# Kernel tuning notes

Hardware: AMD Instinct MI355X
Metric: run time of the kernel (lower is better)

The kernel has to match this reference:

```python
import jax, jax.numpy as jnp
import numpy as np

B, S, D, H, MB = 2, 2048, 2048, 32, 16
HD = D // H          # 64
N = S // MB          # 128 mini-batches
EPS = 1e-5
BASE_LR = 1.0


def setup_inputs() -> dict:
    ks = jax.random.split(jax.random.key(0), 8)
    sc = 1.0 / np.sqrt(D)
    inv = 1.0 / (10000.0 ** (np.arange(0, HD, 2, dtype=np.float64) / HD))
    return {
        "x": jax.random.normal(ks[0], (B, S, D), jnp.float32),
        "pos_frequencies": jnp.asarray(np.outer(np.arange(S), inv), jnp.float32),  # (S, HD//2) rope angles
        "Wq": jax.random.normal(ks[1], (D, D), jnp.float32) * sc,
        "Wk": jax.random.normal(ks[2], (D, D), jnp.float32) * sc,
        "Wv": jax.random.normal(ks[3], (D, D), jnp.float32) * sc,
        "Wo": jax.random.normal(ks[4], (D, D), jnp.float32) * sc,
        "post_gamma": jnp.ones((D,), jnp.float32),
        "post_beta": jnp.zeros((D,), jnp.float32),
        "ilr_W": jax.random.normal(ks[5], (H, 1, D), jnp.float32) * 0.02,  # inner_loop_lr_W
        "ilr_b": jnp.zeros((H, 1), jnp.float32),                            # inner_loop_lr_b
        "lgs": jnp.zeros((MB,), jnp.float32),                               # learnable_gradient_scale
        "ttt_gamma": jnp.ones((H, HD), jnp.float32),                        # ttt_norm_weight
        "ttt_beta": jnp.zeros((H, HD), jnp.float32),                        # ttt_norm_bias
        "W0": jax.random.normal(ks[6], (H, HD, HD), jnp.float32) / np.sqrt(HD),
        "b0": jnp.zeros((H, 1, HD), jnp.float32),
    }


def _rope(x, freqs):
    # x: (B,H,S,HD), freqs: (S,HD//2); rotate interleaved pairs
    cos = jnp.cos(freqs)[None, None]
    sin = jnp.sin(freqs)[None, None]
    x1, x2 = x[..., 0::2], x[..., 1::2]
    return jnp.stack([x1 * cos - x2 * sin, x1 * sin + x2 * cos], -1).reshape(x.shape)


def _ln_fwd(z, g, b):
    mu = z.mean(-1, keepdims=True)
    var = z.var(-1, keepdims=True)
    return g * (z - mu) * jax.lax.rsqrt(var + EPS) + b


def _ln_l2_bwd(z, tgt, g, b):
    # grad of 0.5*||LN(z) - tgt||^2 w.r.t. z (fused LayerNorm backward)
    mu = z.mean(-1, keepdims=True)
    var = z.var(-1, keepdims=True)
    rstd = jax.lax.rsqrt(var + EPS)
    zh = (z - mu) * rstd
    dy = (g * zh + b) - tgt
    dzh = dy * g
    return (dzh - dzh.mean(-1, keepdims=True) - zh * (dzh * zh).mean(-1, keepdims=True)) * rstd


def reference(x, pos_frequencies, Wq, Wk, Wv, Wo, post_gamma, post_beta,
              ilr_W, ilr_b, lgs, ttt_gamma, ttt_beta, W0, b0):
    # projections (torch Linear: x @ W.T), shape (B,H,S,HD)
    q = (x @ Wq.T).reshape(B, S, H, HD).transpose(0, 2, 1, 3)
    k = (x @ Wk.T).reshape(B, S, H, HD).transpose(0, 2, 1, 3)
    v = (x @ Wv.T).reshape(B, S, H, HD).transpose(0, 2, 1, 3)
    q = _rope(q, pos_frequencies)
    k = _rope(k, pos_frequencies)
    v = _rope(v, pos_frequencies)  # module applies RoPE to V too

    # inner-loop learning rates: (B,H,N,1,MB), gradient_scale: (MB,1)
    xr = x.reshape(B, N, MB, D)
    lr = jnp.einsum('bnkd,hod->bhnko', xr, ilr_W) + ilr_b.reshape(1, H, 1, 1, 1)
    lr = BASE_LR * jax.nn.sigmoid(lr).transpose(0, 1, 2, 4, 3) / HD
    gs = jnp.clip(1.0 / jnp.arange(1, MB + 1, dtype=jnp.float32) + lgs, 0.0)
    eta = gs.reshape(1, 1, 1, MB, 1) * lr  # (B,H,N,MB,MB)

    to_n = lambda t: t.reshape(B, H, N, MB, -1).transpose(2, 0, 1, 3, 4)
    Qn, Kn, Vn = to_n(q), to_n(k), to_n(v)           # (N,B,H,MB,HD)
    En = eta.transpose(2, 0, 1, 3, 4)                # (N,B,H,MB,MB)

    g = ttt_gamma.reshape(1, H, 1, HD)
    be = ttt_beta.reshape(1, H, 1, HD)
    W_init = jnp.broadcast_to(W0[None], (B, H, HD, HD))
    b_init = jnp.broadcast_to(b0[None], (B, H, 1, HD))

    def step(carry, inp):
        W, bb = carry
        XQ, XK, XV, E = inp
        Z = XK @ W + bb
        grad = _ln_l2_bwd(Z, XV - XK, g, be)                 # (B,H,MB,HD)
        Attn = jnp.tril(XQ @ XK.swapaxes(-1, -2))            # causal dual form
        b_bar = bb - jnp.tril(E) @ grad
        Z_bar = XQ @ W - (E * Attn) @ grad + b_bar
        last_eta = E[..., -1, :, None]                       # (B,H,MB,1)
        W_new = W - jnp.swapaxes(last_eta * XK, -1, -2) @ grad
        b_new = bb - jnp.sum(last_eta * grad, axis=-2, keepdims=True)
        return (W_new, b_new), XQ + _ln_fwd(Z_bar, g, be)

    _, ys = jax.lax.scan(step, (W_init, b_init), (Qn, Kn, Vn, En))  # ys: (N,B,H,MB,HD)
    out = ys.transpose(1, 0, 3, 2, 4).reshape(B, S, D)

    mu = out.mean(-1, keepdims=True)
    var = out.var(-1, keepdims=True)
    out = post_gamma * (out - mu) * jax.lax.rsqrt(var + EPS) + post_beta
    return out @ Wo.T
```

## Files before the change

### kernel.cpp

```cpp
#include <hip/hip_runtime.h>
#include <hip/hip_bf16.h>
#include <math.h>

#define BB 2
#define SS 2048
#define DD 2048
#define HH 32
#define HDD 64
#define MBB 16
#define NN 128

typedef unsigned short u16;
typedef short bf16x8_t __attribute__((ext_vector_type(8)));
typedef float f32x4_t __attribute__((ext_vector_type(4)));

__device__ __forceinline__ float b2f(u16 u) { return __uint_as_float(((unsigned)u) << 16); }
__device__ __forceinline__ u16 f2b(float f) {
    unsigned u = __float_as_uint(f);
    return (u16)((u + 0x7FFFu + ((u >> 16) & 1u)) >> 16);
}
__device__ __forceinline__ unsigned pk2(float a, float b) {
    return (unsigned)f2b(a) | ((unsigned)f2b(b) << 16);
}
__device__ __forceinline__ unsigned pk2r(u16 a, u16 b) { return (unsigned)a | ((unsigned)b << 16); }
__device__ __forceinline__ float wsum(float x) {
    x += __shfl_xor(x, 32);
    x += __shfl_xor(x, 16);
    x += __shfl_xor(x, 8);
    x += __shfl_xor(x, 4);
    x += __shfl_xor(x, 2);
    x += __shfl_xor(x, 1);
    return x;
}

typedef __attribute__((address_space(3))) unsigned int lds_u32;
typedef __attribute__((address_space(1))) const unsigned int glb_u32;
__device__ __forceinline__ void async_copy16(const void* g, void* l) {
    __builtin_amdgcn_global_load_lds((glb_u32*)g, (lds_u32*)l, 16, 0, 0);
}

__global__ __launch_bounds__(256) void k_cvt5(const float* __restrict__ x, const float* __restrict__ wq,
                                              const float* __restrict__ wk, const float* __restrict__ wv,
                                              const float* __restrict__ wo, u16* __restrict__ xb,
                                              u16* __restrict__ wqb, u16* __restrict__ wkb,
                                              u16* __restrict__ wvb, u16* __restrict__ wob) {
    int sl = blockIdx.y;
    long e = (long)(blockIdx.x * 256 + threadIdx.x) * 4;
    const float* s;
    u16* d;
    if (sl == 0) { s = x; d = xb; }
    else if (sl == 1) { s = x + 4194304; d = xb + 4194304; }
    else if (sl == 2) { s = wq; d = wqb; }
    else if (sl == 3) { s = wk; d = wkb; }
    else if (sl == 4) { s = wv; d = wvb; }
    else { s = wo; d = wob; }
    float4 f = *(const float4*)(s + e);
    uint2 o;
    o.x = pk2(f.x, f.y);
    o.y = pk2(f.z, f.w);
    *(uint2*)(d + e) = o;
}

__global__ void k_trig(const float* __restrict__ pf, float* __restrict__ ct, float* __restrict__ st) {
    int i = blockIdx.x * 256 + threadIdx.x;
    float f = pf[i];
    ct[i] = cosf(f);
    st[i] = sinf(f);
}

template <int EPI>
__global__ __launch_bounds__(256) void k_gemm_bt(const u16* __restrict__ A, const u16* __restrict__ B0,
                                                 const u16* __restrict__ B1, const u16* __restrict__ B2,
                                                 void* __restrict__ C0, void* __restrict__ C1,
                                                 void* __restrict__ C2, int M, int Nn, int K,
                                                 const float* __restrict__ ct, const float* __restrict__ st) {
    __shared__ u16 As[128 * 32];
    __shared__ u16 Bs[128 * 32];
    int z = blockIdx.z;
    const u16* Bm = (z == 0) ? B0 : (z == 1) ? B1 : B2;
    void* Cout = (z == 0) ? C0 : (z == 1) ? C1 : C2;
    int tid = threadIdx.x, lane = tid & 63, wv = tid >> 6;
    int m0 = blockIdx.y * 128, n0 = blockIdx.x * 128;
    int wm = wv >> 1, wn = wv & 1;

    f32x4_t acc[4][4];
    f32x4_t zero = {0.f, 0.f, 0.f, 0.f};
#pragma unroll
    for (int a = 0; a < 4; ++a)
#pragma unroll
        for (int b = 0; b < 4; ++b) acc[a][b] = zero;

    int mrow = lane & 15, qk = (lane >> 4) * 8;
    const int kTiles = K >> 5;
    for (int kt = 0; kt < kTiles; ++kt) {
        __syncthreads();
        int kb = kt << 5;
#pragma unroll
        for (int it = 0; it < 2; ++it) {
            int cb = it * 256 + wv * 64;
            int c = cb + lane;
            const u16* gpA = A + (m0 + (c >> 2)) * K + kb + ((c & 3) << 3);
            async_copy16(gpA, &As[cb << 3]);
            const u16* gpB = Bm + (n0 + (c >> 2)) * K + kb + ((c & 3) << 3);
            async_copy16(gpB, &Bs[cb << 3]);
        }
        asm volatile("s_waitcnt vmcnt(0)" ::: "memory");
        __syncthreads();

        bf16x8_t af[4], bfr[4];
#pragma unroll
        for (int mi = 0; mi < 4; ++mi)
            af[mi] = *(const bf16x8_t*)&As[(wm * 64 + mi * 16 + mrow) * 32 + qk];
#pragma unroll
        for (int ni = 0; ni < 4; ++ni)
            bfr[ni] = *(const bf16x8_t*)&Bs[(wn * 64 + ni * 16 + mrow) * 32 + qk];
#pragma unroll
        for (int mi = 0; mi < 4; ++mi)
#pragma unroll
            for (int ni = 0; ni < 4; ++ni)
                acc[mi][ni] = __builtin_amdgcn_mfma_f32_16x16x32_bf16(af[mi], bfr[ni], acc[mi][ni], 0, 0, 0);
    }

    int col16 = lane & 15, rq = (lane >> 4) * 4;
#pragma unroll
    for (int mi = 0; mi < 4; ++mi) {
#pragma unroll
        for (int ni = 0; ni < 4; ++ni) {
#pragma unroll
            for (int r = 0; r < 4; ++r) {
                int gr = m0 + wm * 64 + mi * 16 + rq + r;
                int gc = n0 + wn * 64 + ni * 16 + col16;
                float val = acc[mi][ni][r];
                if (EPI == 0) {
                    ((float*)Cout)[gr * Nn + gc] = val;
                } else {
                    int b = gr >> 11, s2 = gr & 2047, hh = gc >> 6, hd = gc & 63;
                    int fi = s2 * 32 + (hd >> 1);
                    float c = ct[fi], sn = st[fi];
                    float partner = __shfl_xor(val, 1);
                    float y = (gc & 1) ? (partner * sn + val * c) : (val * c - partner * sn);
                    ((u16*)Cout)[(((b * HH + hh) * SS) + s2) * HDD + hd] = f2b(y);
                }
            }
        }
    }
}

__global__ __launch_bounds__(256) void k_lr(const u16* __restrict__ xb, const float* __restrict__ ilrW,
                                            const float* __restrict__ ilrb, float* __restrict__ lrout) {
    __shared__ u16 xr[4][2048];
    int row0 = blockIdx.x * 4;
    int tid = threadIdx.x, lane = tid & 63, wv = tid >> 6;
    const unsigned* src = (const unsigned*)(xb + row0 * 2048);
    unsigned* dst = (unsigned*)xr;
    for (int i = tid; i < 4096; i += 256) dst[i] = src[i];
    __syncthreads();
    int b = row0 >> 11, s0 = row0 & 2047;
#pragma unroll
    for (int sub = 0; sub < 8; ++sub) {
        int h = wv * 8 + sub;
        const float* wp = ilrW + h * 2048;
        float a0 = 0.f, a1 = 0.f, a2 = 0.f, a3 = 0.f;
        for (int i = 0; i < 16; ++i) {
            int idx = i * 128 + lane * 2;
            float2 w2 = *(const float2*)(wp + idx);
            unsigned p0 = *(const unsigned*)&xr[0][idx];
            unsigned p1 = *(const unsigned*)&xr[1][idx];
            unsigned p2 = *(const unsigned*)&xr[2][idx];
            unsigned p3 = *(const unsigned*)&xr[3][idx];
            a0 += b2f((u16)p0) * w2.x + b2f((u16)(p0 >> 16)) * w2.y;
            a1 += b2f((u16)p1) * w2.x + b2f((u16)(p1 >> 16)) * w2.y;
            a2 += b2f((u16)p2) * w2.x + b2f((u16)(p2 >> 16)) * w2.y;
            a3 += b2f((u16)p3) * w2.x + b2f((u16)(p3 >> 16)) * w2.y;
        }
        a0 = wsum(a0);
        a1 = wsum(a1);
        a2 = wsum(a2);
        a3 = wsum(a3);
        if (lane == 0) {
            float bv = ilrb[h];
            float* op = lrout + ((b * HH + h) * SS) + s0;
            op[0] = (1.0f / (1.0f + expf(-(a0 + bv)))) * (1.0f / 64.0f);
            op[1] = (1.0f / (1.0f + expf(-(a1 + bv)))) * (1.0f / 64.0f);
            op[2] = (1.0f / (1.0f + expf(-(a2 + bv)))) * (1.0f / 64.0f);
            op[3] = (1.0f / (1.0f + expf(-(a3 + bv)))) * (1.0f / 64.0f);
        }
    }
}

__global__ __launch_bounds__(64) void k_scan(const u16* __restrict__ qb, const u16* __restrict__ kb2,
                                             const u16* __restrict__ vb, const float* __restrict__ lrbuf,
                                             const float* __restrict__ lgs, const float* __restrict__ tg,
                                             const float* __restrict__ tb, const float* __restrict__ W0,
                                             const float* __restrict__ b0, u16* __restrict__ ys) {
    __shared__ u16 WbL[64 * 72];
    __shared__ u16 XKT[64 * 40];
    __shared__ u16 GST[64 * 40];
    __shared__ u16 PUL[16 * 40];

    const int bh = blockIdx.x, h = bh & 31, b = bh >> 5;
    const int lane = threadIdx.x & 63;
    const int quad = lane >> 4, col = lane & 15;
    const int base = bh * SS;

    {
        unsigned* p1 = (unsigned*)XKT;
        unsigned* p2 = (unsigned*)GST;
        unsigned* p3 = (unsigned*)PUL;
        for (int i = lane; i < 1280; i += 64) { p1[i] = 0; p2[i] = 0; }
        for (int i = lane; i < 320; i += 64) p3[i] = 0;
    }

    float gd4[4], bd4[4], bbv[4];
#pragma unroll
    for (int tn = 0; tn < 4; ++tn) {
        gd4[tn] = tg[h * 64 + tn * 16 + col];
        bd4[tn] = tb[h * 64 + tn * 16 + col];
        bbv[tn] = b0[h * 64 + tn * 16 + col];
    }
    float gs4[4];
#pragma unroll
    for (int r = 0; r < 4; ++r) {
        int i = quad * 4 + r;
        gs4[r] = fmaxf(1.f / (float)(i + 1) + lgs[i], 0.f);
    }
    const float gs15 = fmaxf(1.f / 16.f + lgs[15], 0.f);

    f32x4_t Wc[4][4];
#pragma unroll
    for (int tm = 0; tm < 4; ++tm)
#pragma unroll
        for (int tn = 0; tn < 4; ++tn)
#pragma unroll
            for (int r = 0; r < 4; ++r)
                Wc[tm][tn][r] = W0[h * 4096 + (tm * 16 + quad * 4 + r) * 64 + tn * 16 + col];

    {
        unsigned* wb32 = (unsigned*)WbL;
#pragma unroll
        for (int tn = 0; tn < 4; ++tn)
#pragma unroll
            for (int tm = 0; tm < 4; ++tm) {
                int a = (tn * 16 + col) * 36 + tm * 4 + quad;
                a = (tn * 16 + col) * 36 + tm * 8 + quad * 2;
                wb32[a] = pk2(Wc[tm][tn][0], Wc[tm][tn][1]);
                wb32[a + 1] = pk2(Wc[tm][tn][2], Wc[tm][tn][3]);
            }
    }

    bf16x8_t ka[2], qa[2];
    float lr4[4];
    u16 kraw[16], vraw[16];
    {
        const u16* kp = kb2 + (base + col) * 64;
        const u16* qp = qb + (base + col) * 64;
#pragma unroll
        for (int kh = 0; kh < 2; ++kh) {
            ka[kh] = *(const bf16x8_t*)(kp + kh * 32 + quad * 8);
            qa[kh] = *(const bf16x8_t*)(qp + kh * 32 + quad * 8);
        }
#pragma unroll
        for (int r = 0; r < 4; ++r) lr4[r] = lrbuf[base + quad * 4 + r];
#pragma unroll
        for (int tn = 0; tn < 4; ++tn)
#pragma unroll
            for (int r = 0; r < 4; ++r) {
                int idx = (base + quad * 4 + r) * 64 + tn * 16 + col;
                kraw[tn * 4 + r] = kb2[idx];
                vraw[tn * 4 + r] = vb[idx];
            }
    }

    const f32x4_t zf = {0.f, 0.f, 0.f, 0.f};

    for (int n = 0; n < NN; ++n) {
        const int s0 = n * 16;

        bf16x8_t wbf[4][2];
#pragma unroll
        for (int tn = 0; tn < 4; ++tn)
#pragma unroll
            for (int kh = 0; kh < 2; ++kh)
                wbf[tn][kh] = *(const bf16x8_t*)&WbL[(tn * 16 + col) * 72 + kh * 32 + quad * 8];

        f32x4_t z[4], xqw[4], attn;
#pragma unroll
        for (int tn = 0; tn < 4; ++tn) {
            z[tn] = __builtin_amdgcn_mfma_f32_16x16x32_bf16(ka[1], wbf[tn][1], zf, 0, 0, 0);
            z[tn] = __builtin_amdgcn_mfma_f32_16x16x32_bf16(ka[0], wbf[tn][0], z[tn], 0, 0, 0);
            xqw[tn] = __builtin_amdgcn_mfma_f32_16x16x32_bf16(qa[1], wbf[tn][1], zf, 0, 0, 0);
            xqw[tn] = __builtin_amdgcn_mfma_f32_16x16x32_bf16(qa[0], wbf[tn][0], xqw[tn], 0, 0, 0);
        }
        attn = __builtin_amdgcn_mfma_f32_16x16x32_bf16(qa[1], ka[1], zf, 0, 0, 0);
        attn = __builtin_amdgcn_mfma_f32_16x16x32_bf16(qa[0], ka[0], attn, 0, 0, 0);

        u16 qraw[16];
#pragma unroll
        for (int tn = 0; tn < 4; ++tn)
#pragma unroll
            for (int r = 0; r < 4; ++r)
                qraw[tn * 4 + r] = qb[(base + s0 + quad * 4 + r) * 64 + tn * 16 + col];

        bf16x8_t nka[2], nqa[2];
        float nlr[4];
        u16 nkraw[16], nvraw[16];
        {
            const int sp = (n + 1 < NN) ? s0 + 16 : s0;
            const u16* kp = kb2 + (base + sp + col) * 64;
            const u16* qp = qb + (base + sp + col) * 64;
#pragma unroll
            for (int kh = 0; kh < 2; ++kh) {
                nka[kh] = *(const bf16x8_t*)(kp + kh * 32 + quad * 8);
                nqa[kh] = *(const bf16x8_t*)(qp + kh * 32 + quad * 8);
            }
#pragma unroll
            for (int r = 0; r < 4; ++r) nlr[r] = lrbuf[base + sp + quad * 4 + r];
#pragma unroll
            for (int tn = 0; tn < 4; ++tn)
#pragma unroll
                for (int r = 0; r < 4; ++r) {
                    int idx = (base + sp + quad * 4 + r) * 64 + tn * 16 + col;
                    nkraw[tn * 4 + r] = kb2[idx];
                    nvraw[tn * 4 + r] = vb[idx];
                }
        }

        {
            unsigned* x32 = (unsigned*)XKT;
#pragma unroll
            for (int tn = 0; tn < 4; ++tn) {
                int a = (tn * 16 + col) * 20 + quad * 2;
                x32[a] = pk2r(kraw[tn * 4 + 0], kraw[tn * 4 + 1]);
                x32[a + 1] = pk2r(kraw[tn * 4 + 2], kraw[tn * 4 + 3]);
            }
        }

#pragma unroll
        for (int tn = 0; tn < 4; ++tn)
#pragma unroll
            for (int r = 0; r < 4; ++r) z[tn][r] += bbv[tn];

        float mu4[4], rstd4[4], m1[4], m2[4];
#pragma unroll
        for (int r = 0; r < 4; ++r) {
            float s1 = z[0][r] + z[1][r] + z[2][r] + z[3][r];
            float s2 = z[0][r] * z[0][r] + z[1][r] * z[1][r] + z[2][r] * z[2][r] + z[3][r] * z[3][r];
#pragma unroll
            for (int m = 1; m <= 8; m <<= 1) { s1 += __shfl_xor(s1, m); s2 += __shfl_xor(s2, m); }
            float mu = s1 * (1.f / 64.f);
            float var = s2 * (1.f / 64.f) - mu * mu;
            mu4[r] = mu;
            rstd4[r] = rsqrtf(var + 1e-5f);
            m1[r] = 0.f;
            m2[r] = 0.f;
        }
#pragma unroll
        for (int tn = 0; tn < 4; ++tn)
#pragma unroll
            for (int r = 0; r < 4; ++r) {
                float zh = (z[tn][r] - mu4[r]) * rstd4[r];
                float tgt = b2f(vraw[tn * 4 + r]) - b2f(kraw[tn * 4 + r]);
                float dzh = (gd4[tn] * zh + bd4[tn] - tgt) * gd4[tn];
                m1[r] += dzh;
                m2[r] += dzh * zh;
            }
#pragma unroll
        for (int r = 0; r < 4; ++r) {
#pragma unroll
            for (int m = 1; m <= 8; m <<= 1) { m1[r] += __shfl_xor(m1[r], m); m2[r] += __shfl_xor(m2[r], m); }
            m1[r] *= (1.f / 64.f);
            m2[r] *= (1.f / 64.f);
        }
        float gS[4][4];
#pragma unroll
        for (int tn = 0; tn < 4; ++tn)
#pragma unroll
            for (int r = 0; r < 4; ++r) {
                float zh = (z[tn][r] - mu4[r]) * rstd4[r];
                float tgt = b2f(vraw[tn * 4 + r]) - b2f(kraw[tn * 4 + r]);
                float dzh = (gd4[tn] * zh + bd4[tn] - tgt) * gd4[tn];
                gS[tn][r] = lr4[r] * ((dzh - m1[r] - zh * m2[r]) * rstd4[r]);
            }
        {
            unsigned* g32 = (unsigned*)GST;
#pragma unroll
            for (int tn = 0; tn < 4; ++tn) {
                int a = (tn * 16 + col) * 20 + quad * 2;
                g32[a] = pk2(gS[tn][0], gS[tn][1]);
                g32[a + 1] = pk2(gS[tn][2], gS[tn][3]);
            }
        }
#pragma unroll
        for (int r = 0; r < 4; ++r) {
            float pv = (col <= quad * 4 + r) ? (1.f + attn[r]) : 0.f;
            PUL[(quad * 4 + r) * 40 + col] = f2b(pv);
        }

        bf16x8_t xkf[4], gsf[4], puf;
#pragma unroll
        for (int t = 0; t < 4; ++t) {
            xkf[t] = *(const bf16x8_t*)&XKT[(t * 16 + col) * 40 + quad * 8];
            gsf[t] = *(const bf16x8_t*)&GST[(t * 16 + col) * 40 + quad * 8];
        }
        puf = *(const bf16x8_t*)&PUL[col * 40 + quad * 8];

#pragma unroll
        for (int tm = 0; tm < 4; ++tm)
#pragma unroll
            for (int tn = 0; tn < 4; ++tn) {
                f32x4_t dw = __builtin_amdgcn_mfma_f32_16x16x32_bf16(xkf[tm], gsf[tn], zf, 0, 0, 0);
#pragma unroll
                for (int r = 0; r < 4; ++r) Wc[tm][tn][r] -= gs15 * dw[r];
            }
        {
            unsigned* wb32 = (unsigned*)WbL;
#pragma unroll
            for (int tn = 0; tn < 4; ++tn)
#pragma unroll
                for (int tm = 0; tm < 4; ++tm) {
                    int a = (tn * 16 + col) * 36 + tm * 8 + quad * 2;
                    wb32[a] = pk2(Wc[tm][tn][0], Wc[tm][tn][1]);
                    wb32[a + 1] = pk2(Wc[tm][tn][2], Wc[tm][tn][3]);
                }
        }

#pragma unroll
        for (int tn = 0; tn < 4; ++tn) {
            f32x4_t pg = __builtin_amdgcn_mfma_f32_16x16x32_bf16(puf, gsf[tn], zf, 0, 0, 0);
#pragma unroll
            for (int r = 0; r < 4; ++r) z[tn][r] = xqw[tn][r] + bbv[tn] - gs4[r] * pg[r];
        }
#pragma unroll
        for (int r = 0; r < 4; ++r) {
            float s1 = z[0][r] + z[1][r] + z[2][r] + z[3][r];
            float s2 = z[0][r] * z[0][r] + z[1][r] * z[1][r] + z[2][r] * z[2][r] + z[3][r] * z[3][r];
#pragma unroll
            for (int m = 1; m <= 8; m <<= 1) { s1 += __shfl_xor(s1, m); s2 += __shfl_xor(s2, m); }
            float mu = s1 * (1.f / 64.f);
            float var = s2 * (1.f / 64.f) - mu * mu;
            mu4[r] = mu;
            rstd4[r] = rsqrtf(var + 1e-5f);
        }
#pragma unroll
        for (int tn = 0; tn < 4; ++tn)
#pragma unroll
            for (int r = 0; r < 4; ++r) {
                float y = b2f(qraw[tn * 4 + r]) + gd4[tn] * (z[tn][r] - mu4[r]) * rstd4[r] + bd4[tn];
                ys[(b * SS + s0 + quad * 4 + r) * DD + h * 64 + tn * 16 + col] = f2b(y);
            }

#pragma unroll
        for (int tn = 0; tn < 4; ++tn) {
            float c = gS[tn][0] + gS[tn][1] + gS[tn][2] + gS[tn][3];
            c += __shfl_xor(c, 16);
            c += __shfl_xor(c, 32);
            bbv[tn] -= gs15 * c;
        }

        ka[0] = nka[0]; ka[1] = nka[1];
        qa[0] = nqa[0]; qa[1] = nqa[1];
#pragma unroll
        for (int r = 0; r < 4; ++r) lr4[r] = nlr[r];
#pragma unroll
        for (int j = 0; j < 16; ++j) { kraw[j] = nkraw[j]; vraw[j] = nvraw[j]; }
    }
}

__global__ __launch_bounds__(256) void k_postln(const u16* __restrict__ ys, const float* __restrict__ pg,
                                                const float* __restrict__ pb, u16* __restrict__ outb) {
    __shared__ float red[8];
    int row = blockIdx.x, tid = threadIdx.x, lane = tid & 63, wv = tid >> 6;
    const u16* rp = ys + row * 2048 + tid * 8;
    uint4 pkd = *(const uint4*)rp;
    float v[8];
    v[0] = b2f((u16)pkd.x); v[1] = b2f((u16)(pkd.x >> 16));
    v[2] = b2f((u16)pkd.y); v[3] = b2f((u16)(pkd.y >> 16));
    v[4] = b2f((u16)pkd.z); v[5] = b2f((u16)(pkd.z >> 16));
    v[6] = b2f((u16)pkd.w); v[7] = b2f((u16)(pkd.w >> 16));
    float s1 = 0.f, s2 = 0.f;
#pragma unroll
    for (int i = 0; i < 8; ++i) { s1 += v[i]; s2 += v[i] * v[i]; }
    s1 = wsum(s1);
    s2 = wsum(s2);
    if (lane == 0) {
        red[wv] = s1;
        red[wv + 4] = s2;
    }
    __syncthreads();
    float S1 = red[0] + red[1] + red[2] + red[3];
    float S2 = red[4] + red[5] + red[6] + red[7];
    float mu = S1 * (1.f / 2048), var = S2 * (1.f / 2048) - mu * mu;
    float rstd = rsqrtf(var + 1e-5f);
    const float4 g0 = *(const float4*)(pg + tid * 8);
    const float4 g1 = *(const float4*)(pg + tid * 8 + 4);
    const float4 b0v = *(const float4*)(pb + tid * 8);
    const float4 b1v = *(const float4*)(pb + tid * 8 + 4);
    float o[8];
    o[0] = g0.x * (v[0] - mu) * rstd + b0v.x;
    o[1] = g0.y * (v[1] - mu) * rstd + b0v.y;
    o[2] = g0.z * (v[2] - mu) * rstd + b0v.z;
    o[3] = g0.w * (v[3] - mu) * rstd + b0v.w;
    o[4] = g1.x * (v[4] - mu) * rstd + b1v.x;
    o[5] = g1.y * (v[5] - mu) * rstd + b1v.y;
    o[6] = g1.z * (v[6] - mu) * rstd + b1v.z;
    o[7] = g1.w * (v[7] - mu) * rstd + b1v.w;
    uint4 po;
    po.x = pk2(o[0], o[1]);
    po.y = pk2(o[2], o[3]);
    po.z = pk2(o[4], o[5]);
    po.w = pk2(o[6], o[7]);
    *(uint4*)(outb + row * 2048 + tid * 8) = po;
}

extern "C" void kernel_launch(void* const* d_in, const int* in_sizes, int n_in,
                              void* d_out, int out_size, void* d_ws, size_t ws_size,
                              hipStream_t stream) {
    const float* x = (const float*)d_in[0];
    const float* pf = (const float*)d_in[1];
    const float* Wq = (const float*)d_in[2];
    const float* Wk = (const float*)d_in[3];
    const float* Wv = (const float*)d_in[4];
    const float* Wo = (const float*)d_in[5];
    const float* pg = (const float*)d_in[6];
    const float* pb = (const float*)d_in[7];
    const float* ilrW = (const float*)d_in[8];
    const float* ilrb = (const float*)d_in[9];
    const float* lgs = (const float*)d_in[10];
    const float* tg = (const float*)d_in[11];
    const float* tb = (const float*)d_in[12];
    const float* W0 = (const float*)d_in[13];
    const float* b0 = (const float*)d_in[14];
    float* out = (float*)d_out;
    char* ws = (char*)d_ws;

    u16* xbf = (u16*)(ws + 0);
    u16* wqb = (u16*)(ws + 16777216);
    u16* wkb = (u16*)(ws + 25165824);
    u16* wvb = (u16*)(ws + 33554432);
    u16* wob = (u16*)(ws + 41943040);
    u16* qbuf = (u16*)(ws + 50331648);
    u16* kbuf = (u16*)(ws + 67108864);
    u16* vbuf = (u16*)(ws + 83886080);
    float* ct = (float*)(ws + 100663296);
    float* st = (float*)(ws + 100925440);
    float* lrb = (float*)(ws + 101187584);
    u16* ysb = (u16*)(ws + 101711872);
    u16* lnb = (u16*)(ws + 0);

    k_cvt5<<<dim3(4096, 6), 256, 0, stream>>>(x, Wq, Wk, Wv, Wo, xbf, wqb, wkb, wvb, wob);
    k_trig<<<256, 256, 0, stream>>>(pf, ct, st);

    k_gemm_bt<1><<<dim3(16, 32, 3), 256, 0, stream>>>(xbf, wqb, wkb, wvb, qbuf, kbuf, vbuf,
                                                      4096, 2048, 2048, ct, st);

    k_lr<<<1024, 256, 0, stream>>>(xbf, ilrW, ilrb, lrb);

    k_scan<<<64, 64, 0, stream>>>(qbuf, kbuf, vbuf, lrb, lgs, tg, tb, W0, b0, ysb);

    k_postln<<<4096, 256, 0, stream>>>(ysb, pg, pb, lnb);
    k_gemm_bt<0><<<dim3(16, 32, 1), 256, 0, stream>>>(lnb, wob, wob, wob, out, out, out,
                                                      4096, 2048, 2048, nullptr, nullptr);
}
```

Before: 853.4 us.

## Pack eight scan heads per workgroup and pad XKT/GST LDS stride

The TTT scan kernel previously launched 64 single-wave workgroups, one per (batch, head). It now launches 8 workgroups of 512 threads, each wave owning a private slice of LDS for its head. The XKT/GST row stride also changes from 40 to 36 elements, and reads are split into two 4-element loads, apparently to reduce LDS bank conflicts. Packing waves onto fewer CUs may cut launch or scheduling overhead, but it concentrates all 64 serial scans onto 8 CUs. That risks contention for MFMA, LDS and VGPR resources and could lengthen the latency-bound serial loop.

```diff
diff --git a/kernel.cpp b/kernel.cpp
--- a/kernel.cpp
+++ b/kernel.cpp
@@ -12,6 +12,7 @@
 
 typedef unsigned short u16;
 typedef short bf16x8_t __attribute__((ext_vector_type(8)));
+typedef short bf16x4_t __attribute__((ext_vector_type(4)));
 typedef float f32x4_t __attribute__((ext_vector_type(4)));
 
 __device__ __forceinline__ float b2f(u16 u) { return __uint_as_float(((unsigned)u) << 16); }
@@ -188,26 +189,32 @@
     }
 }
 
-__global__ __launch_bounds__(64) void k_scan(const u16* __restrict__ qb, const u16* __restrict__ kb2,
-                                             const u16* __restrict__ vb, const float* __restrict__ lrbuf,
-                                             const float* __restrict__ lgs, const float* __restrict__ tg,
-                                             const float* __restrict__ tb, const float* __restrict__ W0,
-                                             const float* __restrict__ b0, u16* __restrict__ ys) {
-    __shared__ u16 WbL[64 * 72];
-    __shared__ u16 XKT[64 * 40];
-    __shared__ u16 GST[64 * 40];
-    __shared__ u16 PUL[16 * 40];
-
-    const int bh = blockIdx.x, h = bh & 31, b = bh >> 5;
+__global__ __launch_bounds__(512) void k_scan(const u16* __restrict__ qb, const u16* __restrict__ kb2,
+                                              const u16* __restrict__ vb, const float* __restrict__ lrbuf,
+                                              const float* __restrict__ lgs, const float* __restrict__ tg,
+                                              const float* __restrict__ tb, const float* __restrict__ W0,
+                                              const float* __restrict__ b0, u16* __restrict__ ys) {
+    __shared__ u16 WbL[8][64 * 72];
+    __shared__ u16 XKT[8][64 * 36];
+    __shared__ u16 GST[8][64 * 36];
+    __shared__ u16 PUL[8][16 * 40];
+
+    const int w = threadIdx.x >> 6;
+    const int bh = blockIdx.x * 8 + w, h = bh & 31, b = bh >> 5;
     const int lane = threadIdx.x & 63;
     const int quad = lane >> 4, col = lane & 15;
     const int base = bh * SS;
 
+    u16* const WbLw = WbL[w];
+    u16* const XKTw = XKT[w];
+    u16* const GSTw = GST[w];
+    u16* const PULw = PUL[w];
+
     {
-        unsigned* p1 = (unsigned*)XKT;
-        unsigned* p2 = (unsigned*)GST;
-        unsigned* p3 = (unsigned*)PUL;
-        for (int i = lane; i < 1280; i += 64) { p1[i] = 0; p2[i] = 0; }
+        unsigned* p1 = (unsigned*)XKTw;
+        unsigned* p2 = (unsigned*)GSTw;
+        unsigned* p3 = (unsigned*)PULw;
+        for (int i = lane; i < 1152; i += 64) { p1[i] = 0; p2[i] = 0; }
         for (int i = lane; i < 320; i += 64) p3[i] = 0;
     }
 
@@ -236,13 +243,12 @@
                 Wc[tm][tn][r] = W0[h * 4096 + (tm * 16 + quad * 4 + r) * 64 + tn * 16 + col];
 
     {
-        unsigned* wb32 = (unsigned*)WbL;
+        unsigned* wb32 = (unsigned*)WbLw;
 #pragma unroll
         for (int tn = 0; tn < 4; ++tn)
 #pragma unroll
             for (int tm = 0; tm < 4; ++tm) {
-                int a = (tn * 16 + col) * 36 + tm * 4 + quad;
-                a = (tn * 16 + col) * 36 + tm * 8 + quad * 2;
+                int a = (tn * 16 + col) * 36 + tm * 8 + quad * 2;
                 wb32[a] = pk2(Wc[tm][tn][0], Wc[tm][tn][1]);
                 wb32[a + 1] = pk2(Wc[tm][tn][2], Wc[tm][tn][3]);
             }
@@ -281,7 +287,7 @@
         for (int tn = 0; tn < 4; ++tn)
 #pragma unroll
             for (int kh = 0; kh < 2; ++kh)
-                wbf[tn][kh] = *(const bf16x8_t*)&WbL[(tn * 16 + col) * 72 + kh * 32 + quad * 8];
+                wbf[tn][kh] = *(const bf16x8_t*)&WbLw[(tn * 16 + col) * 72 + kh * 32 + quad * 8];
 
         f32x4_t z[4], xqw[4], attn;
 #pragma unroll
@@ -326,10 +332,10 @@
         }
 
         {
-            unsigned* x32 = (unsigned*)XKT;
+            unsigned* x32 = (unsigned*)XKTw;
 #pragma unroll
             for (int tn = 0; tn < 4; ++tn) {
-                int a = (tn * 16 + col) * 20 + quad * 2;
+                int a = (tn * 16 + col) * 18 + quad * 2;
                 x32[a] = pk2r(kraw[tn * 4 + 0], kraw[tn * 4 + 1]);
                 x32[a + 1] = pk2r(kraw[tn * 4 + 2], kraw[tn * 4 + 3]);
             }
@@ -382,10 +388,10 @@
                 gS[tn][r] = lr4[r] * ((dzh - m1[r] - zh * m2[r]) * rstd4[r]);
             }
         {
-            unsigned* g32 = (unsigned*)GST;
+            unsigned* g32 = (unsigned*)GSTw;
 #pragma unroll
             for (int tn = 0; tn < 4; ++tn) {
-                int a = (tn * 16 + col) * 20 + quad * 2;
+                int a = (tn * 16 + col) * 18 + quad * 2;
                 g32[a] = pk2(gS[tn][0], gS[tn][1]);
                 g32[a + 1] = pk2(gS[tn][2], gS[tn][3]);
             }
@@ -393,16 +399,20 @@
 #pragma unroll
         for (int r = 0; r < 4; ++r) {
             float pv = (col <= quad * 4 + r) ? (1.f + attn[r]) : 0.f;
-            PUL[(quad * 4 + r) * 40 + col] = f2b(pv);
+            PULw[(quad * 4 + r) * 40 + col] = f2b(pv);
         }
 
         bf16x8_t xkf[4], gsf[4], puf;
 #pragma unroll
         for (int t = 0; t < 4; ++t) {
-            xkf[t] = *(const bf16x8_t*)&XKT[(t * 16 + col) * 40 + quad * 8];
-            gsf[t] = *(const bf16x8_t*)&GST[(t * 16 + col) * 40 + quad * 8];
-        }
-        puf = *(const bf16x8_t*)&PUL[col * 40 + quad * 8];
+            bf16x4_t xl = *(const bf16x4_t*)&XKTw[(t * 16 + col) * 36 + quad * 8];
+            bf16x4_t xh = *(const bf16x4_t*)&XKTw[(t * 16 + col) * 36 + quad * 8 + 4];
+            xkf[t] = __builtin_shufflevector(xl, xh, 0, 1, 2, 3, 4, 5, 6, 7);
+            bf16x4_t gl = *(const bf16x4_t*)&GSTw[(t * 16 + col) * 36 + quad * 8];
+            bf16x4_t gh = *(const bf16x4_t*)&GSTw[(t * 16 + col) * 36 + quad * 8 + 4];
+            gsf[t] = __builtin_shufflevector(gl, gh, 0, 1, 2, 3, 4, 5, 6, 7);
+        }
+        puf = *(const bf16x8_t*)&PULw[col * 40 + quad * 8];
 
 #pragma unroll
         for (int tm = 0; tm < 4; ++tm)
@@ -413,7 +423,7 @@
                 for (int r = 0; r < 4; ++r) Wc[tm][tn][r] -= gs15 * dw[r];
             }
         {
-            unsigned* wb32 = (unsigned*)WbL;
+            unsigned* wb32 = (unsigned*)WbLw;
 #pragma unroll
             for (int tn = 0; tn < 4; ++tn)
 #pragma unroll
@@ -555,7 +565,7 @@
 
     k_lr<<<1024, 256, 0, stream>>>(xbf, ilrW, ilrb, lrb);
 
-    k_scan<<<64, 64, 0, stream>>>(qbuf, kbuf, vbuf, lrb, lgs, tg, tb, W0, b0, ysb);
+    k_scan<<<dim3(8), 512, 0, stream>>>(qbuf, kbuf, vbuf, lrb, lgs, tg, tb, W0, b0, ysb);
 
     k_postln<<<4096, 256, 0, stream>>>(ysb, pg, pb, lnb);
     k_gemm_bt<0><<<dim3(16, 32, 1), 256, 0, stream>>>(lnb, wob, wob, wob, out, out, out,
```

Measured after the change: 1.215 ms. +42.4%, slower.

## Permute head-dim layout for vectorized scan loads/stores and hoist LDS fragment reloads

Applied to the files above, without the earlier changes.

Adds a permuted head-dimension layout (d -> (d&15)*4 + d>>4) for Q, K and V so the sequential scan kernel can fetch each thread's 4 values with one vector load and write ys as ushort4. V is produced permuted directly in the QKV GEMM epilogue, Q and K get a separate permute pass, and Wo columns plus post-LN gamma/beta are permuted to match so the output GEMM stays consistent. The scan also moves the XK LDS staging and W fragment reloads to the end of each iteration for the next step. The aim is to cut scalar global traffic on the latency-bound 64-block scan, at the cost of an extra prep kernel and workspace aliasing.

```diff
diff --git a/kernel.cpp b/kernel.cpp
--- a/kernel.cpp
+++ b/kernel.cpp
@@ -39,6 +39,7 @@
     __builtin_amdgcn_global_load_lds((glb_u32*)g, (lds_u32*)l, 16, 0, 0);
 }
 
+
 __global__ __launch_bounds__(256) void k_cvt5(const float* __restrict__ x, const float* __restrict__ wq,
                                               const float* __restrict__ wk, const float* __restrict__ wv,
                                               const float* __restrict__ wo, u16* __restrict__ xb,
@@ -46,14 +47,25 @@
                                               u16* __restrict__ wvb, u16* __restrict__ wob) {
     int sl = blockIdx.y;
     long e = (long)(blockIdx.x * 256 + threadIdx.x) * 4;
+    if (sl == 5) {
+        long n = e >> 11;
+        int cin = (int)(e & 2047);
+        int hd0 = (cin >> 6) * 64 + ((cin & 63) >> 2);
+        const float* src = wo + n * 2048 + hd0;
+        float f0 = src[0], f1 = src[16], f2 = src[32], f3 = src[48];
+        uint2 o;
+        o.x = pk2(f0, f1);
+        o.y = pk2(f2, f3);
+        *(uint2*)(wob + e) = o;
+        return;
+    }
     const float* s;
     u16* d;
     if (sl == 0) { s = x; d = xb; }
     else if (sl == 1) { s = x + 4194304; d = xb + 4194304; }
     else if (sl == 2) { s = wq; d = wqb; }
     else if (sl == 3) { s = wk; d = wkb; }
-    else if (sl == 4) { s = wv; d = wvb; }
-    else { s = wo; d = wob; }
+    else { s = wv; d = wvb; }
     float4 f = *(const float4*)(s + e);
     uint2 o;
     o.x = pk2(f.x, f.y);
@@ -66,6 +78,30 @@
     float f = pf[i];
     ct[i] = cosf(f);
     st[i] = sinf(f);
+}
+
+__global__ void k_ppg(const float* __restrict__ pg, const float* __restrict__ pb,
+                      float* __restrict__ pgp, float* __restrict__ pbp) {
+    int i = blockIdx.x * 256 + threadIdx.x;
+    int h = i >> 6, o = i & 63;
+    int src = h * 64 + (o >> 2) + (o & 3) * 16;
+    pgp[i] = pg[src];
+    pbp[i] = pb[src];
+}
+
+__global__ __launch_bounds__(256) void k_prep(const u16* __restrict__ qb, const u16* __restrict__ kb,
+                                              u16* __restrict__ qc, u16* __restrict__ kc) {
+    long row = (long)blockIdx.x * 256 + threadIdx.x;
+    const u16* src = (blockIdx.y == 0 ? qb : kb) + row * 64;
+    u16* dst = (blockIdx.y == 0 ? qc : kc) + row * 64;
+    u16 v[64];
+#pragma unroll
+    for (int i = 0; i < 8; ++i) *(uint4*)&v[i * 8] = *(const uint4*)(src + i * 8);
+    u16 o[64];
+#pragma unroll
+    for (int d = 0; d < 64; ++d) o[(d & 15) * 4 + (d >> 4)] = v[d];
+#pragma unroll
+    for (int i = 0; i < 8; ++i) *(uint4*)(dst + i * 8) = *(uint4*)&o[i * 8];
 }
 
 template <int EPI>
@@ -139,7 +175,8 @@
                     float c = ct[fi], sn = st[fi];
                     float partner = __shfl_xor(val, 1);
                     float y = (gc & 1) ? (partner * sn + val * c) : (val * c - partner * sn);
-                    ((u16*)Cout)[(((b * HH + hh) * SS) + s2) * HDD + hd] = f2b(y);
+                    int po = (z == 2) ? ((hd & 15) * 4 + (hd >> 4)) : hd;
+                    ((u16*)Cout)[(((b * HH + hh) * SS) + s2) * HDD + po] = f2b(y);
                 }
             }
         }
@@ -188,11 +225,12 @@
     }
 }
 
-__global__ __launch_bounds__(64) void k_scan(const u16* __restrict__ qb, const u16* __restrict__ kb2,
-                                             const u16* __restrict__ vb, const float* __restrict__ lrbuf,
-                                             const float* __restrict__ lgs, const float* __restrict__ tg,
-                                             const float* __restrict__ tb, const float* __restrict__ W0,
-                                             const float* __restrict__ b0, u16* __restrict__ ys) {
+__global__ __launch_bounds__(64, 1) void k_scan(const u16* __restrict__ qb, const u16* __restrict__ kb2,
+                                                const u16* __restrict__ qc, const u16* __restrict__ kc,
+                                                const u16* __restrict__ vc, const float* __restrict__ lrbuf,
+                                                const float* __restrict__ lgs, const float* __restrict__ tg,
+                                                const float* __restrict__ tb, const float* __restrict__ W0,
+                                                const float* __restrict__ b0, u16* __restrict__ ys) {
     __shared__ u16 WbL[64 * 72];
     __shared__ u16 XKT[64 * 40];
     __shared__ u16 GST[64 * 40];
@@ -241,8 +279,7 @@
         for (int tn = 0; tn < 4; ++tn)
 #pragma unroll
             for (int tm = 0; tm < 4; ++tm) {
-                int a = (tn * 16 + col) * 36 + tm * 4 + quad;
-                a = (tn * 16 + col) * 36 + tm * 8 + quad * 2;
+                int a = (tn * 16 + col) * 36 + tm * 8 + quad * 2;
                 wb32[a] = pk2(Wc[tm][tn][0], Wc[tm][tn][1]);
                 wb32[a + 1] = pk2(Wc[tm][tn][2], Wc[tm][tn][3]);
             }
@@ -250,7 +287,7 @@
 
     bf16x8_t ka[2], qa[2];
     float lr4[4];
-    u16 kraw[16], vraw[16];
+    u16 kraw[16], vraw[16], qraw[16];
     {
         const u16* kp = kb2 + (base + col) * 64;
         const u16* qp = qb + (base + col) * 64;
@@ -262,26 +299,40 @@
 #pragma unroll
         for (int r = 0; r < 4; ++r) lr4[r] = lrbuf[base + quad * 4 + r];
 #pragma unroll
+        for (int r = 0; r < 4; ++r) {
+            long ro = (long)(base + quad * 4 + r) * 64 + col * 4;
+            ushort4 tk = *(const ushort4*)(kc + ro);
+            ushort4 tv = *(const ushort4*)(vc + ro);
+            ushort4 tq = *(const ushort4*)(qc + ro);
+            kraw[r] = tk.x; kraw[4 + r] = tk.y; kraw[8 + r] = tk.z; kraw[12 + r] = tk.w;
+            vraw[r] = tv.x; vraw[4 + r] = tv.y; vraw[8 + r] = tv.z; vraw[12 + r] = tv.w;
+            qraw[r] = tq.x; qraw[4 + r] = tq.y; qraw[8 + r] = tq.z; qraw[12 + r] = tq.w;
+        }
+    }
+
+    bf16x8_t xkf[4], wbf[4][2];
+    {
+        unsigned* x32 = (unsigned*)XKT;
+#pragma unroll
+        for (int tn = 0; tn < 4; ++tn) {
+            int a = (tn * 16 + col) * 20 + quad * 2;
+            x32[a] = pk2r(kraw[tn * 4 + 0], kraw[tn * 4 + 1]);
+            x32[a + 1] = pk2r(kraw[tn * 4 + 2], kraw[tn * 4 + 3]);
+        }
+#pragma unroll
+        for (int t = 0; t < 4; ++t)
+            xkf[t] = *(const bf16x8_t*)&XKT[(t * 16 + col) * 40 + quad * 8];
+#pragma unroll
         for (int tn = 0; tn < 4; ++tn)
 #pragma unroll
-            for (int r = 0; r < 4; ++r) {
-                int idx = (base + quad * 4 + r) * 64 + tn * 16 + col;
-                kraw[tn * 4 + r] = kb2[idx];
-                vraw[tn * 4 + r] = vb[idx];
-            }
+            for (int kh = 0; kh < 2; ++kh)
+                wbf[tn][kh] = *(const bf16x8_t*)&WbL[(tn * 16 + col) * 72 + kh * 32 + quad * 8];
     }
 
     const f32x4_t zf = {0.f, 0.f, 0.f, 0.f};
 
     for (int n = 0; n < NN; ++n) {
         const int s0 = n * 16;
-
-        bf16x8_t wbf[4][2];
-#pragma unroll
-        for (int tn = 0; tn < 4; ++tn)
-#pragma unroll
-            for (int kh = 0; kh < 2; ++kh)
-                wbf[tn][kh] = *(const bf16x8_t*)&WbL[(tn * 16 + col) * 72 + kh * 32 + quad * 8];
 
         f32x4_t z[4], xqw[4], attn;
 #pragma unroll
@@ -294,16 +345,15 @@
         attn = __builtin_amdgcn_mfma_f32_16x16x32_bf16(qa[1], ka[1], zf, 0, 0, 0);
         attn = __builtin_amdgcn_mfma_f32_16x16x32_bf16(qa[0], ka[0], attn, 0, 0, 0);
 
-        u16 qraw[16];
-#pragma unroll
-        for (int tn = 0; tn < 4; ++tn)
-#pragma unroll
-            for (int r = 0; r < 4; ++r)
-                qraw[tn * 4 + r] = qb[(base + s0 + quad * 4 + r) * 64 + tn * 16 + col];
+#pragma unroll
+        for (int r = 0; r < 4; ++r) {
+            float pv = (col <= quad * 4 + r) ? (1.f + attn[r]) : 0.f;
+            PUL[(quad * 4 + r) * 40 + col] = f2b(pv);
+        }
 
         bf16x8_t nka[2], nqa[2];
         float nlr[4];
-        u16 nkraw[16], nvraw[16];
+        u16 nkraw[16], nvraw[16], nqraw[16];
         {
             const int sp = (n + 1 < NN) ? s0 + 16 : s0;
             const u16* kp = kb2 + (base + sp + col) * 64;
@@ -316,22 +366,14 @@
 #pragma unroll
             for (int r = 0; r < 4; ++r) nlr[r] = lrbuf[base + sp + quad * 4 + r];
 #pragma unroll
-            for (int tn = 0; tn < 4; ++tn)
-#pragma unroll
-                for (int r = 0; r < 4; ++r) {
-                    int idx = (base + sp + quad * 4 + r) * 64 + tn * 16 + col;
-                    nkraw[tn * 4 + r] = kb2[idx];
-                    nvraw[tn * 4 + r] = vb[idx];
-                }
-        }
-
-        {
-            unsigned* x32 = (unsigned*)XKT;
-#pragma unroll
-            for (int tn = 0; tn < 4; ++tn) {
-                int a = (tn * 16 + col) * 20 + quad * 2;
-                x32[a] = pk2r(kraw[tn * 4 + 0], kraw[tn * 4 + 1]);
-                x32[a + 1] = pk2r(kraw[tn * 4 + 2], kraw[tn * 4 + 3]);
+            for (int r = 0; r < 4; ++r) {
+                long ro = (long)(base + sp + quad * 4 + r) * 64 + col * 4;
+                ushort4 tk = *(const ushort4*)(kc + ro);
+                ushort4 tv = *(const ushort4*)(vc + ro);
+                ushort4 tq = *(const ushort4*)(qc + ro);
+                nkraw[r] = tk.x; nkraw[4 + r] = tk.y; nkraw[8 + r] = tk.z; nkraw[12 + r] = tk.w;
+                nvraw[r] = tv.x; nvraw[4 + r] = tv.y; nvraw[8 + r] = tv.z; nvraw[12 + r] = tv.w;
+                nqraw[r] = tq.x; nqraw[4 + r] = tq.y; nqraw[8 + r] = tq.z; nqraw[12 + r] = tq.w;
             }
         }
 
@@ -390,18 +432,11 @@
                 g32[a + 1] = pk2(gS[tn][2], gS[tn][3]);
             }
         }
-#pragma unroll
-        for (int r = 0; r < 4; ++r) {
-            float pv = (col <= quad * 4 + r) ? (1.f + attn[r]) : 0.f;
-            PUL[(quad * 4 + r) * 40 + col] = f2b(pv);
-        }
-
-        bf16x8_t xkf[4], gsf[4], puf;
-#pragma unroll
-        for (int t = 0; t < 4; ++t) {
-            xkf[t] = *(const bf16x8_t*)&XKT[(t * 16 + col) * 40 + quad * 8];
+
+        bf16x8_t gsf[4], puf;
+#pragma unroll
+        for (int t = 0; t < 4; ++t)
             gsf[t] = *(const bf16x8_t*)&GST[(t * 16 + col) * 40 + quad * 8];
-        }
         puf = *(const bf16x8_t*)&PUL[col * 40 + quad * 8];
 
 #pragma unroll
@@ -442,12 +477,15 @@
             rstd4[r] = rsqrtf(var + 1e-5f);
         }
 #pragma unroll
-        for (int tn = 0; tn < 4; ++tn)
-#pragma unroll
-            for (int r = 0; r < 4; ++r) {
-                float y = b2f(qraw[tn * 4 + r]) + gd4[tn] * (z[tn][r] - mu4[r]) * rstd4[r] + bd4[tn];
-                ys[(b * SS + s0 + quad * 4 + r) * DD + h * 64 + tn * 16 + col] = f2b(y);
-            }
+        for (int r = 0; r < 4; ++r) {
+            ushort4 yv;
+            float y0 = b2f(qraw[0 * 4 + r]) + gd4[0] * (z[0][r] - mu4[r]) * rstd4[r] + bd4[0];
+            float y1 = b2f(qraw[1 * 4 + r]) + gd4[1] * (z[1][r] - mu4[r]) * rstd4[r] + bd4[1];
+            float y2 = b2f(qraw[2 * 4 + r]) + gd4[2] * (z[2][r] - mu4[r]) * rstd4[r] + bd4[2];
+            float y3 = b2f(qraw[3 * 4 + r]) + gd4[3] * (z[3][r] - mu4[r]) * rstd4[r] + bd4[3];
+            yv.x = f2b(y0); yv.y = f2b(y1); yv.z = f2b(y2); yv.w = f2b(y3);
+            *(ushort4*)(ys + (long)(b * SS + s0 + quad * 4 + r) * DD + h * 64 + col * 4) = yv;
+        }
 
 #pragma unroll
         for (int tn = 0; tn < 4; ++tn) {
@@ -457,12 +495,30 @@
             bbv[tn] -= gs15 * c;
         }
 
+        {
+            unsigned* x32 = (unsigned*)XKT;
+#pragma unroll
+            for (int tn = 0; tn < 4; ++tn) {
+                int a = (tn * 16 + col) * 20 + quad * 2;
+                x32[a] = pk2r(nkraw[tn * 4 + 0], nkraw[tn * 4 + 1]);
+                x32[a + 1] = pk2r(nkraw[tn * 4 + 2], nkraw[tn * 4 + 3]);
+            }
+#pragma unroll
+            for (int t = 0; t < 4; ++t)
+                xkf[t] = *(const bf16x8_t*)&XKT[(t * 16 + col) * 40 + quad * 8];
+#pragma unroll
+            for (int tn = 0; tn < 4; ++tn)
+#pragma unroll
+                for (int kh = 0; kh < 2; ++kh)
+                    wbf[tn][kh] = *(const bf16x8_t*)&WbL[(tn * 16 + col) * 72 + kh * 32 + quad * 8];
+        }
+
         ka[0] = nka[0]; ka[1] = nka[1];
         qa[0] = nqa[0]; qa[1] = nqa[1];
 #pragma unroll
         for (int r = 0; r < 4; ++r) lr4[r] = nlr[r];
 #pragma unroll
-        for (int j = 0; j < 16; ++j) { kraw[j] = nkraw[j]; vraw[j] = nvraw[j]; }
+        for (int j = 0; j < 16; ++j) { kraw[j] = nkraw[j]; vraw[j] = nvraw[j]; qraw[j] = nqraw[j]; }
     }
 }
 
@@ -545,19 +601,26 @@
     float* st = (float*)(ws + 100925440);
     float* lrb = (float*)(ws + 101187584);
     u16* ysb = (u16*)(ws + 101711872);
+    float* pgp = (float*)(ws + 118489088);
+    float* pbp = (float*)(ws + 118497280);
+    u16* qc = (u16*)(ws + 16777216);
+    u16* kc = (u16*)(ws + 0);
     u16* lnb = (u16*)(ws + 0);
 
     k_cvt5<<<dim3(4096, 6), 256, 0, stream>>>(x, Wq, Wk, Wv, Wo, xbf, wqb, wkb, wvb, wob);
     k_trig<<<256, 256, 0, stream>>>(pf, ct, st);
+    k_ppg<<<8, 256, 0, stream>>>(pg, pb, pgp, pbp);
 
     k_gemm_bt<1><<<dim3(16, 32, 3), 256, 0, stream>>>(xbf, wqb, wkb, wvb, qbuf, kbuf, vbuf,
                                                       4096, 2048, 2048, ct, st);
 
     k_lr<<<1024, 256, 0, stream>>>(xbf, ilrW, ilrb, lrb);
 
-    k_scan<<<64, 64, 0, stream>>>(qbuf, kbuf, vbuf, lrb, lgs, tg, tb, W0, b0, ysb);
-
-    k_postln<<<4096, 256, 0, stream>>>(ysb, pg, pb, lnb);
+    k_prep<<<dim3(512, 2), 256, 0, stream>>>(qbuf, kbuf, qc, kc);
+
+    k_scan<<<64, 64, 0, stream>>>(qbuf, kbuf, qc, kc, vbuf, lrb, lgs, tg, tb, W0, b0, ysb);
+
+    k_postln<<<4096, 256, 0, stream>>>(ysb, pgp, pbp, lnb);
     k_gemm_bt<0><<<dim3(16, 32, 1), 256, 0, stream>>>(lnb, wob, wob, wob, out, out, out,
                                                       4096, 2048, 2048, nullptr, nullptr);
 }
```

Measured after the change: 876.3 us. +2.7%, slower.
